# Kernel optimization log

Measured on AMD Instinct MI355X. Metric: run time of the kernel, lower is better.

## Reference

```python
import jax, jax.numpy as jnp
import numpy as np

D_MODEL = 256
D_STATE = 128          # d_model // 2
D_CONV = 4
EXPAND = 4
D_INNER = EXPAND * D_MODEL  # 1024
DT_RANK = (D_MODEL + 15) // 16  # 16
N_HEADS = 8
D_FF = 4 * D_MODEL
EPS = 1e-6


def layer_norm(x, a, b):
    # torch LayerNorm-like but with unbiased std (ddof=1) per the source
    mean = jnp.mean(x, axis=-1, keepdims=True)
    d = x.shape[-1]
    var = jnp.sum((x - mean) ** 2, axis=-1, keepdims=True) / (d - 1)
    std = jnp.sqrt(var)
    return a * (x - mean) / (std + EPS) + b


def silu(x):
    return x * jax.nn.sigmoid(x)


def mamba(x, in_proj_w, conv_w, conv_b, x_proj_w, dt_proj_w, dt_proj_b, A_log, Dp, out_proj_w):
    B, L, _ = x.shape
    xz = jnp.einsum('bld,ed->ble', x, in_proj_w)  # (B,L,2*D_INNER)
    xi, z = xz[..., :D_INNER], xz[..., D_INNER:]
    # causal depthwise conv1d over L
    xp = jnp.pad(xi, ((0, 0), (D_CONV - 1, 0), (0, 0)))
    u = conv_b
    for k in range(D_CONV):
        u = u + xp[:, k:k + L, :] * conv_w[:, k]
    u = silu(u)  # (B,L,D_INNER)
    dbl = jnp.einsum('bld,ed->ble', u, x_proj_w)  # (B,L,DT_RANK+2*D_STATE)
    dt = dbl[..., :DT_RANK]
    Bm = dbl[..., DT_RANK:DT_RANK + D_STATE]
    Cm = dbl[..., DT_RANK + D_STATE:]
    dt = jax.nn.softplus(jnp.einsum('blr,dr->bld', dt, dt_proj_w) + dt_proj_b)  # (B,L,D_INNER)
    A = -jnp.exp(A_log)  # (D_INNER, D_STATE)
    dA = jnp.exp(jnp.einsum('bld,dn->bldn', dt, A))          # (B,L,Din,N)
    dBu = jnp.einsum('bld,bln,bld->bldn', dt, Bm, u)          # (B,L,Din,N)

    def step(h, inp):
        dA_t, dBu_t, C_t = inp
        h = dA_t * h + dBu_t                    # (B,Din,N)
        y = jnp.einsum('bdn,bn->bd', h, C_t)    # (B,Din)
        return h, y

    h0 = jnp.zeros((B, D_INNER, D_STATE), dtype=x.dtype)
    _, ys = jax.lax.scan(step, h0, (jnp.swapaxes(dA, 0, 1), jnp.swapaxes(dBu, 0, 1), jnp.swapaxes(Cm, 0, 1)))
    y = jnp.swapaxes(ys, 0, 1) + u * Dp  # (B,L,Din)
    y = y * silu(z)
    return jnp.einsum('ble,de->bld', y, out_proj_w)


def cross_attention(q_in, kv_in, mask, wq_w, wq_b, wk_w, wk_b, wv_w, wv_b, wo_w, wo_b):
    B, Lq, _ = q_in.shape
    Lk = kv_in.shape[1]
    dk = D_MODEL // N_HEADS
    q = (jnp.einsum('bld,ed->ble', q_in, wq_w) + wq_b).reshape(B, Lq, N_HEADS, dk).transpose(0, 2, 1, 3)
    k = (jnp.einsum('bld,ed->ble', kv_in, wk_w) + wk_b).reshape(B, Lk, N_HEADS, dk).transpose(0, 2, 1, 3)
    v = (jnp.einsum('bld,ed->ble', kv_in, wv_w) + wv_b).reshape(B, Lk, N_HEADS, dk).transpose(0, 2, 1, 3)
    scores = jnp.einsum('bhqd,bhkd->bhqk', q, k) / np.sqrt(dk)
    # mask: (B,1,Lk) bool -> broadcast (B,1,1,Lk)
    scores = jnp.where(mask[:, None, :, :], scores, jnp.finfo(scores.dtype).min)
    p = jax.nn.softmax(scores, axis=-1)
    o = jnp.einsum('bhqk,bhkd->bhqd', p, v).transpose(0, 2, 1, 3).reshape(B, Lq, D_MODEL)
    return jnp.einsum('ble,de->bld', o, wo_w) + wo_b


def setup_inputs() -> dict:
    key = jax.random.key(0)
    ks = jax.random.split(key, 24)
    s = 0.02
    B, L, Lm = 2, 512, 512
    inp = {
        'x': jax.random.normal(ks[0], (B, L, D_MODEL), jnp.float32),
        'memory': jax.random.normal(ks[1], (B, Lm, D_MODEL), jnp.float32),
        'src_mask': jnp.ones((B, 1, Lm), bool),
        'tgt_mask': jnp.ones((B, 1, L), bool),
        # mamba params
        'in_proj_w': jax.random.normal(ks[2], (2 * D_INNER, D_MODEL)) * s,
        'conv_w': jax.random.normal(ks[3], (D_INNER, D_CONV)) * s,
        'conv_b': jnp.zeros((D_INNER,)),
        'x_proj_w': jax.random.normal(ks[4], (DT_RANK + 2 * D_STATE, D_INNER)) * s,
        'dt_proj_w': jax.random.normal(ks[5], (D_INNER, DT_RANK)) * s,
        'dt_proj_b': jnp.log(jnp.expm1(0.01)) * jnp.ones((D_INNER,)),
        'A_log': jnp.log(jnp.broadcast_to(jnp.arange(1, D_STATE + 1, dtype=jnp.float32), (D_INNER, D_STATE))),
        'Dp': jnp.ones((D_INNER,)),
        'out_proj_w': jax.random.normal(ks[6], (D_MODEL, D_INNER)) * s,
        # norms
        'norm1_a': jnp.ones((D_MODEL,)), 'norm1_b': jnp.zeros((D_MODEL,)),
        'norm2_a': jnp.ones((D_MODEL,)), 'norm2_b': jnp.zeros((D_MODEL,)),
        'norm3_a': jnp.ones((D_MODEL,)), 'norm3_b': jnp.zeros((D_MODEL,)),
        # cross attention
        'wq_w': jax.random.normal(ks[7], (D_MODEL, D_MODEL)) * s, 'wq_b': jnp.zeros((D_MODEL,)),
        'wk_w': jax.random.normal(ks[8], (D_MODEL, D_MODEL)) * s, 'wk_b': jnp.zeros((D_MODEL,)),
        'wv_w': jax.random.normal(ks[9], (D_MODEL, D_MODEL)) * s, 'wv_b': jnp.zeros((D_MODEL,)),
        'wo_w': jax.random.normal(ks[10], (D_MODEL, D_MODEL)) * s, 'wo_b': jnp.zeros((D_MODEL,)),
        # ffn
        'w1_w': jax.random.normal(ks[11], (D_FF, D_MODEL)) * s, 'w1_b': jnp.zeros((D_FF,)),
        'w2_w': jax.random.normal(ks[12], (D_MODEL, D_FF)) * s, 'w2_b': jnp.zeros((D_MODEL,)),
    }
    return inp


def reference(x, memory, src_mask, tgt_mask,
              in_proj_w, conv_w, conv_b, x_proj_w, dt_proj_w, dt_proj_b, A_log, Dp, out_proj_w,
              norm1_a, norm1_b, norm2_a, norm2_b, norm3_a, norm3_b,
              wq_w, wq_b, wk_w, wk_b, wv_w, wv_b, wo_w, wo_b,
              w1_w, w1_b, w2_w, w2_b):
    # self mamba block (pre-norm, residual); dropout = 0
    h = x + mamba(layer_norm(x, norm1_a, norm1_b), in_proj_w, conv_w, conv_b,
                  x_proj_w, dt_proj_w, dt_proj_b, A_log, Dp, out_proj_w)
    # cross attention block
    h = h + cross_attention(layer_norm(h, norm2_a, norm2_b), memory, src_mask,
                            wq_w, wq_b, wk_w, wk_b, wv_w, wv_b, wo_w, wo_b)
    # ffn block
    hn = layer_norm(h, norm3_a, norm3_b)
    ff = jnp.einsum('blf,df->bld', jax.nn.relu(jnp.einsum('bld,fd->blf', hn, w1_w) + w1_b), w2_w) + w2_b
    return h + ff
```

## Files before the change

kernel.cpp:

```cpp
#include <hip/hip_runtime.h>
#include <hip/hip_bf16.h>

#define B_SZ 2
#define L_SEQ 512
#define D_MODEL 256
#define D_STATE 128
#define D_CONV 4
#define D_INNER 1024
#define DT_RANK 16
#define N_HEADS 8
#define DK 32
#define D_FF 1024
#define R_TOT (B_SZ * L_SEQ)
#define DBL_LD (DT_RANK + 2 * D_STATE)
#define NSEG 16
#define SEGL 32
#define DPB 4

typedef __hip_bfloat16 bf16;
typedef __attribute__((ext_vector_type(8))) short short8;
typedef __attribute__((ext_vector_type(4))) float floatx4;

__device__ inline float fexp(float x) { return __expf(x); }
__device__ inline float fexp2(float x) { return __builtin_amdgcn_exp2f(x); }
__device__ inline float frcp(float x) { return __builtin_amdgcn_rcpf(x); }
__device__ inline float silu_f(float x) { return x * frcp(1.f + fexp(-x)); }
__device__ inline float softplus_f(float x) { return (x > 20.f) ? x : __logf(1.f + fexp(x)); }
__device__ inline float bf2f(unsigned short u) { return __uint_as_float(((unsigned)u) << 16); }

__device__ inline float dpp_sum64(float x) {
    x += __int_as_float(__builtin_amdgcn_update_dpp(0, __float_as_int(x), 0x111, 0xf, 0xf, true));
    x += __int_as_float(__builtin_amdgcn_update_dpp(0, __float_as_int(x), 0x112, 0xf, 0xf, true));
    x += __int_as_float(__builtin_amdgcn_update_dpp(0, __float_as_int(x), 0x114, 0xf, 0xf, true));
    x += __int_as_float(__builtin_amdgcn_update_dpp(0, __float_as_int(x), 0x118, 0xf, 0xf, true));
    x += __int_as_float(__builtin_amdgcn_update_dpp(0, __float_as_int(x), 0x142, 0xf, 0xf, true));
    x += __int_as_float(__builtin_amdgcn_update_dpp(0, __float_as_int(x), 0x143, 0xf, 0xf, true));
    return x;
}

__device__ inline float swz_xor16(float x) {
    return __int_as_float(__builtin_amdgcn_ds_swizzle(__float_as_int(x), 0x401F));
}
__device__ inline float swz_xor8(float x) {
    return __int_as_float(__builtin_amdgcn_ds_swizzle(__float_as_int(x), 0x201F));
}

#define S_MEM 262144
#define S_INW 524288
#define S_XPW 278528
#define S_OPW 262144
#define S_WQ  65536
#define S_WK  65536
#define S_WV  65536
#define S_WO  65536
#define S_W1  262144
#define S_W2  262144
#define S_TOT (S_MEM+S_INW+S_XPW+S_OPW+S_WQ+S_WK+S_WV+S_WO+S_W1+S_W2)
#define PACK_BLKS ((S_TOT + 255) / 256)
#define Z1_F4 (4 * R_TOT * D_MODEL / 4)
#define Z2_F4 (R_TOT * D_MODEL / 4)
#define Z3_F4 (R_TOT * DBL_LD / 4)
#define ZERO_BLKS ((Z1_F4 + Z2_F4 + Z3_F4 + 255) / 256)

__global__ __launch_bounds__(256) void pack_ln1(
    const float* __restrict__ s0, const float* __restrict__ s1,
    const float* __restrict__ s2, const float* __restrict__ s3,
    const float* __restrict__ s4, const float* __restrict__ s5,
    const float* __restrict__ s6, const float* __restrict__ s7,
    const float* __restrict__ s8, const float* __restrict__ s9,
    bf16* __restrict__ dst,
    const float* __restrict__ X, const float* __restrict__ a,
    const float* __restrict__ bvec, bf16* __restrict__ ln1b,
    float* __restrict__ zero1, float* __restrict__ zero2,
    float* __restrict__ zero3)
{
    __shared__ float r1[256], r2[256];
    if (blockIdx.x < PACK_BLKS) {
        const long i = (long)blockIdx.x * 256 + threadIdx.x;
        if (i >= S_TOT) return;
        const long off[11] = {0, S_MEM, S_MEM+S_INW, S_MEM+S_INW+S_XPW,
            S_MEM+S_INW+S_XPW+S_OPW, S_MEM+S_INW+S_XPW+S_OPW+S_WQ,
            S_MEM+S_INW+S_XPW+S_OPW+S_WQ+S_WK,
            S_MEM+S_INW+S_XPW+S_OPW+S_WQ+S_WK+S_WV,
            S_MEM+S_INW+S_XPW+S_OPW+S_WQ+S_WK+S_WV+S_WO,
            S_MEM+S_INW+S_XPW+S_OPW+S_WQ+S_WK+S_WV+S_WO+S_W1, S_TOT};
        const float* srcs[10] = {s0,s1,s2,s3,s4,s5,s6,s7,s8,s9};
        int seg = 0;
#pragma unroll
        for (int k = 1; k < 10; ++k) if (i >= off[k]) seg = k;
        dst[i] = __float2bfloat16(srcs[seg][i - off[seg]]);
    } else if (blockIdx.x < PACK_BLKS + R_TOT) {
        const int row = blockIdx.x - PACK_BLKS;
        const int t = threadIdx.x;
        const float v = X[(long)row * D_MODEL + t];
        r1[t] = v;
        r2[t] = v * v;
        __syncthreads();
        for (int s = 128; s > 0; s >>= 1) {
            if (t < s) { r1[t] += r1[t + s]; r2[t] += r2[t + s]; }
            __syncthreads();
        }
        const float mean = r1[0] * (1.f / 256.f);
        const float var = (r2[0] - 256.f * mean * mean) * (1.f / 255.f);
        const float sd = sqrtf(fmaxf(var, 0.f));
        const float o = a[t] * (v - mean) / (sd + 1e-6f) + bvec[t];
        ln1b[(long)row * D_MODEL + t] = __float2bfloat16(o);
    } else {
        const long i4 = (long)(blockIdx.x - PACK_BLKS - R_TOT) * 256 + threadIdx.x;
        const float4 z = {0.f, 0.f, 0.f, 0.f};
        if (i4 < Z1_F4)                      *(float4*)&zero1[i4 * 4] = z;
        else if (i4 < Z1_F4 + Z2_F4)          *(float4*)&zero2[(i4 - Z1_F4) * 4] = z;
        else if (i4 < Z1_F4 + Z2_F4 + Z3_F4)  *(float4*)&zero3[(i4 - Z1_F4 - Z2_F4) * 4] = z;
    }
}

template <int EPI>
__global__ __launch_bounds__(256) void mfma_gemm(
    const bf16* __restrict__ A, const bf16* __restrict__ W, int K,
    float* __restrict__ C, bf16* __restrict__ Cb, int ldc,
    const float* __restrict__ bias, const float* __restrict__ res,
    int M, int N)
{
    const int wave = threadIdx.x >> 6;
    const int lane = threadIdx.x & 63;
    const int row16 = lane & 15;
    const int quad  = lane >> 4;
    const int bm = blockIdx.y * 64 + wave * 16;
    const int bn = blockIdx.x * 64;

    floatx4 acc[4];
#pragma unroll
    for (int t = 0; t < 4; ++t) acc[t] = (floatx4){0.f, 0.f, 0.f, 0.f};

    const long arow = (long)(bm + row16) * K;
    for (int k0 = 0; k0 < K; k0 += 32) {
        const short8 av = *(const short8*)(A + arow + k0 + quad * 8);
#pragma unroll
        for (int t = 0; t < 4; ++t) {
            const int gn = bn + t * 16 + row16;
            short8 bv = {0,0,0,0,0,0,0,0};
            if (gn < N) bv = *(const short8*)(W + (long)gn * K + k0 + quad * 8);
            acc[t] = __builtin_amdgcn_mfma_f32_16x16x32_bf16(av, bv, acc[t], 0, 0, 0);
        }
    }

#pragma unroll
    for (int t = 0; t < 4; ++t) {
        const int gn = bn + t * 16 + row16;
        if (gn >= N) continue;
        const float bs = bias ? bias[gn] : 0.f;
#pragma unroll
        for (int r = 0; r < 4; ++r) {
            const int gm = bm + quad * 4 + r;
            float v = acc[t][r] + bs;
            if (EPI == 1) v = fmaxf(v, 0.f);
            const long ci = (long)gm * ldc + gn;
            if (res) v += res[ci];
            if (C)  C[ci] = v;
            if (Cb) Cb[ci] = __float2bfloat16(v);
        }
    }
}

template <int SK>
__global__ __launch_bounds__(256) void splitk_gemm(
    const bf16* __restrict__ A, const bf16* __restrict__ W, int K,
    float* __restrict__ C, int ldc,
    const float* __restrict__ bias, const float* __restrict__ res,
    int M, int N)
{
    const int wave = threadIdx.x >> 6;
    const int lane = threadIdx.x & 63;
    const int row16 = lane & 15;
    const int quad  = lane >> 4;
    const int bm = blockIdx.y * 64 + wave * 16;
    const int bn = blockIdx.x * 64;
    const int kz = blockIdx.z;
    const int ksl = K / SK;
    const int kbeg = kz * ksl;

    floatx4 acc[4];
#pragma unroll
    for (int t = 0; t < 4; ++t) acc[t] = (floatx4){0.f, 0.f, 0.f, 0.f};

    const long arow = (long)(bm + row16) * K;
    for (int k0 = kbeg; k0 < kbeg + ksl; k0 += 32) {
        const short8 av = *(const short8*)(A + arow + k0 + quad * 8);
#pragma unroll
        for (int t = 0; t < 4; ++t) {
            const int gn = bn + t * 16 + row16;
            short8 bv = {0,0,0,0,0,0,0,0};
            if (gn < N) bv = *(const short8*)(W + (long)gn * K + k0 + quad * 8);
            acc[t] = __builtin_amdgcn_mfma_f32_16x16x32_bf16(av, bv, acc[t], 0, 0, 0);
        }
    }

#pragma unroll
    for (int t = 0; t < 4; ++t) {
        const int gn = bn + t * 16 + row16;
        if (gn >= N) continue;
        const float bs = (kz == 0 && bias) ? bias[gn] : 0.f;
#pragma unroll
        for (int r = 0; r < 4; ++r) {
            const int gm = bm + quad * 4 + r;
            float v = acc[t][r] + bs;
            const long ci = (long)gm * ldc + gn;
            if (kz == 0 && res) v += res[ci];
            atomicAdd(&C[ci], v);
        }
    }
}

__global__ __launch_bounds__(256) void xproj_kv_gemm(
    const bf16* __restrict__ ub, const bf16* __restrict__ XPWb,
    float* __restrict__ dbl,
    const bf16* __restrict__ memb, const bf16* __restrict__ WKb,
    const bf16* __restrict__ WVb,
    const float* __restrict__ WKB, const float* __restrict__ WVB,
    float* __restrict__ kb, float* __restrict__ vb)
{
    const int wave = threadIdx.x >> 6;
    const int lane = threadIdx.x & 63;
    const int row16 = lane & 15;
    const int quad  = lane >> 4;
    const int bm = blockIdx.y * 64 + wave * 16;
    const int bn = blockIdx.x * 64;
    const int z = blockIdx.z;

    const bf16* A; const bf16* W; const float* bias; float* C;
    int K, N, ldc, kbeg, ksl;
    if (z < 4) {
        A = ub; W = XPWb; bias = nullptr; C = dbl;
        K = D_INNER; N = DBL_LD; ldc = DBL_LD;
        ksl = D_INNER / 4; kbeg = z * ksl;
    } else {
        if (bn >= D_MODEL) return;
        const int zz = z - 4;
        const int which = zz >> 1;
        const int kz = zz & 1;
        A = memb; W = which ? WVb : WKb;
        bias = (kz == 0) ? (which ? WVB : WKB) : nullptr;
        C = which ? vb : kb;
        K = D_MODEL; N = D_MODEL; ldc = D_MODEL;
        ksl = D_MODEL / 2; kbeg = kz * ksl;
    }

    floatx4 acc[4];
#pragma unroll
    for (int t = 0; t < 4; ++t) acc[t] = (floatx4){0.f, 0.f, 0.f, 0.f};

    const long arow = (long)(bm + row16) * K;
    for (int k0 = kbeg; k0 < kbeg + ksl; k0 += 32) {
        const short8 av = *(const short8*)(A + arow + k0 + quad * 8);
#pragma unroll
        for (int t = 0; t < 4; ++t) {
            const int gn = bn + t * 16 + row16;
            short8 bv = {0,0,0,0,0,0,0,0};
            if (gn < N) bv = *(const short8*)(W + (long)gn * K + k0 + quad * 8);
            acc[t] = __builtin_amdgcn_mfma_f32_16x16x32_bf16(av, bv, acc[t], 0, 0, 0);
        }
    }

#pragma unroll
    for (int t = 0; t < 4; ++t) {
        const int gn = bn + t * 16 + row16;
        if (gn >= N) continue;
        const float bs = bias ? bias[gn] : 0.f;
#pragma unroll
        for (int r = 0; r < 4; ++r) {
            const int gm = bm + quad * 4 + r;
            atomicAdd(&C[(long)gm * ldc + gn], acc[t][r] + bs);
        }
    }
}

__global__ __launch_bounds__(256) void q_gemm(
    const bf16* __restrict__ ln2b, const bf16* __restrict__ WQb,
    const float* __restrict__ WQB, float* __restrict__ qb)
{
    const int wave = threadIdx.x >> 6;
    const int lane = threadIdx.x & 63;
    const int row16 = lane & 15;
    const int quad  = lane >> 4;
    const int bm = blockIdx.y * 64 + wave * 16;
    const int bn = blockIdx.x * 64;
    const int kz = blockIdx.z;
    const int kbeg = kz * (D_MODEL / 2);

    floatx4 acc[4];
#pragma unroll
    for (int t = 0; t < 4; ++t) acc[t] = (floatx4){0.f, 0.f, 0.f, 0.f};

    const long arow = (long)(bm + row16) * D_MODEL;
    for (int k0 = kbeg; k0 < kbeg + D_MODEL / 2; k0 += 32) {
        const short8 av = *(const short8*)(ln2b + arow + k0 + quad * 8);
#pragma unroll
        for (int t = 0; t < 4; ++t) {
            const int gn = bn + t * 16 + row16;
            const short8 bv = *(const short8*)(WQb + (long)gn * D_MODEL + k0 + quad * 8);
            acc[t] = __builtin_amdgcn_mfma_f32_16x16x32_bf16(av, bv, acc[t], 0, 0, 0);
        }
    }
#pragma unroll
    for (int t = 0; t < 4; ++t) {
        const int gn = bn + t * 16 + row16;
        const float bs = (kz == 0) ? WQB[gn] : 0.f;
#pragma unroll
        for (int r = 0; r < 4; ++r) {
            const int gm = bm + quad * 4 + r;
            atomicAdd(&qb[(long)gm * D_MODEL + gn], acc[t][r] + bs);
        }
    }
}

__global__ __launch_bounds__(256) void gemm16_ln(
    const bf16* __restrict__ A, const bf16* __restrict__ W, int K,
    const float* __restrict__ bias, const float* __restrict__ res,
    float* __restrict__ Cf,
    const float* __restrict__ lna, const float* __restrict__ lnb,
    bf16* __restrict__ lnout)
{
    __shared__ float tile[16][264];
    __shared__ float red1[16][16];
    __shared__ float red2[16][16];
    const int w = threadIdx.x >> 6;
    const int lane = threadIdx.x & 63;
    const int row16 = lane & 15;
    const int quad  = lane >> 4;
    const int bm = blockIdx.x * 16;

    floatx4 acc[4];
#pragma unroll
    for (int t = 0; t < 4; ++t) acc[t] = (floatx4){0.f, 0.f, 0.f, 0.f};

    const long arow = (long)(bm + row16) * K;
    for (int k0 = 0; k0 < K; k0 += 32) {
        const short8 av = *(const short8*)(A + arow + k0 + quad * 8);
#pragma unroll
        for (int t = 0; t < 4; ++t) {
            const int gn = w * 64 + t * 16 + row16;
            const short8 bv = *(const short8*)(W + (long)gn * K + k0 + quad * 8);
            acc[t] = __builtin_amdgcn_mfma_f32_16x16x32_bf16(av, bv, acc[t], 0, 0, 0);
        }
    }

#pragma unroll
    for (int t = 0; t < 4; ++t) {
        const int gn = w * 64 + t * 16 + row16;
        const float bs = bias ? bias[gn] : 0.f;
#pragma unroll
        for (int r = 0; r < 4; ++r) {
            const int gm = bm + quad * 4 + r;
            float v = acc[t][r] + bs;
            const long ci = (long)gm * D_MODEL + gn;
            if (res) v += res[ci];
            Cf[ci] = v;
            tile[quad * 4 + r][gn] = v;
        }
    }
    __syncthreads();

    const int r = threadIdx.x >> 4;
    const int g = threadIdx.x & 15;
    float s = 0.f, q = 0.f;
#pragma unroll
    for (int i = 0; i < 16; ++i) {
        const float x = tile[r][g * 16 + i];
        s += x; q += x * x;
    }
    red1[r][g] = s; red2[r][g] = q;
    __syncthreads();
    float ts = 0.f, tq = 0.f;
#pragma unroll
    for (int i = 0; i < 16; ++i) { ts += red1[r][i]; tq += red2[r][i]; }
    const float mean = ts * (1.f / 256.f);
    const float var = (tq - 256.f * mean * mean) * (1.f / 255.f);
    const float sd = sqrtf(fmaxf(var, 0.f));
    const long rowbase = (long)(bm + r) * D_MODEL;
#pragma unroll
    for (int i = 0; i < 16; ++i) {
        const int c = g * 16 + i;
        const float o = lna[c] * (tile[r][c] - mean) / (sd + 1e-6f) + lnb[c];
        lnout[rowbase + c] = __float2bfloat16(o);
    }
}

__global__ __launch_bounds__(256) void ln_kernel(
    const float* __restrict__ x, const float* __restrict__ a,
    const float* __restrict__ bvec, bf16* __restrict__ out)
{
    const int row = blockIdx.x;
    const int t = threadIdx.x;
    const float v = x[(long)row * D_MODEL + t];
    __shared__ float r1[256], r2[256];
    r1[t] = v;
    r2[t] = v * v;
    __syncthreads();
    for (int s = 128; s > 0; s >>= 1) {
        if (t < s) { r1[t] += r1[t + s]; r2[t] += r2[t + s]; }
        __syncthreads();
    }
    const float mean = r1[0] * (1.f / 256.f);
    const float var = (r2[0] - 256.f * mean * mean) * (1.f / 255.f);
    const float sd = sqrtf(fmaxf(var, 0.f));
    const float o = a[t] * (v - mean) / (sd + 1e-6f) + bvec[t];
    out[(long)row * D_MODEL + t] = __float2bfloat16(o);
}

__global__ __launch_bounds__(256) void dt_gemm_T(
    const float* __restrict__ A , const float* __restrict__ W ,
    const float* __restrict__ bias, float* __restrict__ dtT)
{
    __shared__ float As[DT_RANK][65];
    __shared__ float Bs[DT_RANK][65];
    __shared__ float Ct[64][65];
    const int bm = blockIdx.y * 64;
    const int bn = blockIdx.x * 64;
    const int tid = threadIdx.x;
    const int tx = tid & 15;
    const int ty = tid >> 4;
    const int r = tid >> 2;
    const int kk = (tid & 3) * 4;
#pragma unroll
    for (int q = 0; q < 4; ++q) {
        As[kk + q][r] = A[(long)(bm + r) * DBL_LD + kk + q];
        Bs[kk + q][r] = W[(long)(bn + r) * DT_RANK + kk + q];
    }
    __syncthreads();
    float acc[4][4] = {};
#pragma unroll
    for (int k = 0; k < DT_RANK; ++k) {
        float a[4], bv[4];
#pragma unroll
        for (int i = 0; i < 4; ++i) a[i] = As[k][ty * 4 + i];
#pragma unroll
        for (int j = 0; j < 4; ++j) bv[j] = Bs[k][tx * 4 + j];
#pragma unroll
        for (int i = 0; i < 4; ++i)
#pragma unroll
            for (int j = 0; j < 4; ++j)
                acc[i][j] = fmaf(a[i], bv[j], acc[i][j]);
    }
#pragma unroll
    for (int i = 0; i < 4; ++i)
#pragma unroll
        for (int j = 0; j < 4; ++j)
            Ct[tx * 4 + j][ty * 4 + i] = softplus_f(acc[i][j] + bias[bn + tx * 4 + j]);
    __syncthreads();
    const int b = bm >> 9;
    const int l0 = bm & 511;
    const int r2 = tid >> 4;
    const int c4 = (tid & 15) * 4;
#pragma unroll
    for (int q = 0; q < 4; ++q) {
        const int dl = r2 + q * 16;
        float4 v = {Ct[dl][c4], Ct[dl][c4 + 1], Ct[dl][c4 + 2], Ct[dl][c4 + 3]};
        *(float4*)&dtT[((long)(b * D_INNER + bn + dl) << 9) + l0 + c4] = v;
    }
}

__global__ __launch_bounds__(256) void conv_silu_T(
    const bf16* __restrict__ xz, const float* __restrict__ cw,
    const float* __restrict__ cb, bf16* __restrict__ ub, float* __restrict__ uT)
{
    __shared__ float t[64][65];
    const int db = blockIdx.x;
    const int lb = blockIdx.y;
    const int b  = blockIdx.z;
    const int tid = threadIdx.x;
    const int r  = tid >> 4;
    const int c4 = (tid & 15) * 4;
    const int d0 = db * 64 + c4;

    const float4 cb4 = *(const float4*)&cb[d0];
    float cwa[4][4];
#pragma unroll
    for (int i = 0; i < 4; ++i) {
        const float4 w = *(const float4*)&cw[(d0 + i) * 4];
        cwa[i][0] = w.x; cwa[i][1] = w.y; cwa[i][2] = w.z; cwa[i][3] = w.w;
    }

#pragma unroll
    for (int q = 0; q < 4; ++q) {
        const int ll = r + q * 16;
        const int l = lb * 64 + ll;
        float s0 = cb4.x, s1 = cb4.y, s2 = cb4.z, s3 = cb4.w;
#pragma unroll
        for (int k = 0; k < D_CONV; ++k) {
            const int ls = l - 3 + k;
            if (ls >= 0) {
                const ushort4 xv = *(const ushort4*)&xz[((long)(b * L_SEQ + ls)) * (2 * D_INNER) + d0];
                s0 = fmaf(bf2f(xv.x), cwa[0][k], s0);
                s1 = fmaf(bf2f(xv.y), cwa[1][k], s1);
                s2 = fmaf(bf2f(xv.z), cwa[2][k], s2);
                s3 = fmaf(bf2f(xv.w), cwa[3][k], s3);
            }
        }
        s0 = silu_f(s0); s1 = silu_f(s1); s2 = silu_f(s2); s3 = silu_f(s3);
        bf16 b0 = __float2bfloat16(s0), b1 = __float2bfloat16(s1);
        bf16 b2 = __float2bfloat16(s2), b3 = __float2bfloat16(s3);
        ushort4 pk;
        pk.x = *reinterpret_cast<unsigned short*>(&b0);
        pk.y = *reinterpret_cast<unsigned short*>(&b1);
        pk.z = *reinterpret_cast<unsigned short*>(&b2);
        pk.w = *reinterpret_cast<unsigned short*>(&b3);
        *reinterpret_cast<ushort4*>(ub + ((long)(b * L_SEQ + l)) * D_INNER + d0) = pk;
        t[c4 + 0][ll] = s0; t[c4 + 1][ll] = s1;
        t[c4 + 2][ll] = s2; t[c4 + 3][ll] = s3;
    }
    __syncthreads();
#pragma unroll
    for (int q = 0; q < 4; ++q) {
        const int dl = r + q * 16;
        float4 v = {t[dl][c4], t[dl][c4 + 1], t[dl][c4 + 2], t[dl][c4 + 3]};
        *(float4*)&uT[((long)(b * D_INNER + db * 64 + dl) << 9) + lb * 64 + c4] = v;
    }
}

__global__ __launch_bounds__(1024) void scan_fused(
    const float* __restrict__ dtT, const float* __restrict__ uT,
    const float* __restrict__ dbl, const float* __restrict__ A_log,
    float* __restrict__ ysT)
{
    const int b  = blockIdx.x >> 8;
    const int d0 = (blockIdx.x & 255) * DPB;
    const int w = threadIdx.x >> 6;
    const int lane = threadIdx.x & 63;
    const int n0 = lane * 2;

    __shared__ float Sh[NSEG][DPB][D_STATE];
    __shared__ float Ph[NSEG][DPB][D_STATE];

    float An0[DPB], An1[DPB];
#pragma unroll
    for (int di = 0; di < DPB; ++di) {
        An0[di] = -fexp(A_log[(long)(d0 + di) * D_STATE + n0]) * 1.44269504f;
        An1[di] = -fexp(A_log[(long)(d0 + di) * D_STATE + n0 + 1]) * 1.44269504f;
    }

    const float* blp = dbl + ((long)(b * L_SEQ + w * SEGL)) * DBL_LD + DT_RANK + n0;
    const float* clp = blp + D_STATE;
    const long tbase = ((long)(b * D_INNER + d0) << 9) + w * SEGL;

    if (w < NSEG - 1) {
        float h0[DPB] = {}, h1[DPB] = {}, sdt[DPB] = {};
        for (int s = 0; s < SEGL / 8; ++s) {
            float2 Bv[8];
#pragma unroll
            for (int j = 0; j < 8; ++j)
                Bv[j] = *(const float2*)(blp + (long)(s * 8 + j) * DBL_LD);
#pragma unroll
            for (int di = 0; di < DPB; ++di) {
                const float* dtp = dtT + tbase + ((long)di << 9) + s * 8;
                const float* up  = uT  + tbase + ((long)di << 9) + s * 8;
                const float4 dt0 = *(const float4*)dtp;
                const float4 dt1 = *(const float4*)(dtp + 4);
                const float4 u0  = *(const float4*)up;
                const float4 u1  = *(const float4*)(up + 4);
                const float dts[8] = {dt0.x, dt0.y, dt0.z, dt0.w, dt1.x, dt1.y, dt1.z, dt1.w};
                const float us[8]  = {u0.x,  u0.y,  u0.z,  u0.w,  u1.x,  u1.y,  u1.z,  u1.w};
#pragma unroll
                for (int j = 0; j < 8; ++j) {
                    const float dtv = dts[j];
                    sdt[di] += dtv;
                    const float dtu = dtv * us[j];
                    h0[di] = fmaf(fexp2(dtv * An0[di]), h0[di], dtu * Bv[j].x);
                    h1[di] = fmaf(fexp2(dtv * An1[di]), h1[di], dtu * Bv[j].y);
                }
            }
        }
#pragma unroll
        for (int di = 0; di < DPB; ++di) {
            Sh[w][di][n0]     = h0[di];
            Sh[w][di][n0 + 1] = h1[di];
            Ph[w][di][n0]     = fexp2(An0[di] * sdt[di]);
            Ph[w][di][n0 + 1] = fexp2(An1[di] * sdt[di]);
        }
    }
    __syncthreads();

    float h0[DPB] = {}, h1[DPB] = {};
    for (int s = 0; s < w; ++s) {
#pragma unroll
        for (int di = 0; di < DPB; ++di) {
            h0[di] = fmaf(Ph[s][di][n0],     h0[di], Sh[s][di][n0]);
            h1[di] = fmaf(Ph[s][di][n0 + 1], h1[di], Sh[s][di][n0 + 1]);
        }
    }

    const int bpa = (lane ^ 32) << 2;
    const bool lo32 = lane < 32;
    const bool b16 = (lane & 16) != 0;
    const bool b8  = (lane & 8) != 0;
    const int g = lane >> 3;
    const bool wl = (lane & 7) == 7;

    for (int s = 0; s < SEGL / 8; ++s) {
        float2 Bv[8], Cv[8];
#pragma unroll
        for (int j = 0; j < 8; ++j) {
            Bv[j] = *(const float2*)(blp + (long)(s * 8 + j) * DBL_LD);
            Cv[j] = *(const float2*)(clp + (long)(s * 8 + j) * DBL_LD);
        }
#pragma unroll
        for (int di = 0; di < DPB; ++di) {
            const float* dtp = dtT + tbase + ((long)di << 9) + s * 8;
            const float* up  = uT  + tbase + ((long)di << 9) + s * 8;
            const float4 dt0 = *(const float4*)dtp;
            const float4 dt1 = *(const float4*)(dtp + 4);
            const float4 u0  = *(const float4*)up;
            const float4 u1  = *(const float4*)(up + 4);
            const float dts[8] = {dt0.x, dt0.y, dt0.z, dt0.w, dt1.x, dt1.y, dt1.z, dt1.w};
            const float us[8]  = {u0.x,  u0.y,  u0.z,  u0.w,  u1.x,  u1.y,  u1.z,  u1.w};
            float yp[8];
#pragma unroll
            for (int j = 0; j < 8; ++j) {
                const float dtv = dts[j];
                const float dtu = dtv * us[j];
                h0[di] = fmaf(fexp2(dtv * An0[di]), h0[di], dtu * Bv[j].x);
                h1[di] = fmaf(fexp2(dtv * An1[di]), h1[di], dtu * Bv[j].y);
                yp[j] = fmaf(h0[di], Cv[j].x, h1[di] * Cv[j].y);
            }
            float z0[4];
#pragma unroll
            for (int j = 0; j < 4; ++j) {
                const float t = lo32 ? yp[j]     : yp[j + 4];
                const float u = lo32 ? yp[j + 4] : yp[j];
                z0[j] = t + __int_as_float(
                    __builtin_amdgcn_ds_bpermute(bpa, __float_as_int(u)));
            }
            float z1[2];
#pragma unroll
            for (int j = 0; j < 2; ++j) {
                const float t = b16 ? z0[j + 2] : z0[j];
                const float u = b16 ? z0[j]     : z0[j + 2];
                z1[j] = t + swz_xor16(u);
            }
            float z2;
            {
                const float t = b8 ? z1[1] : z1[0];
                const float u = b8 ? z1[0] : z1[1];
                z2 = t + swz_xor8(u);
            }
            z2 += __int_as_float(__builtin_amdgcn_update_dpp(0, __float_as_int(z2), 0x111, 0xf, 0xf, true));
            z2 += __int_as_float(__builtin_amdgcn_update_dpp(0, __float_as_int(z2), 0x112, 0xf, 0xf, true));
            z2 += __int_as_float(__builtin_amdgcn_update_dpp(0, __float_as_int(z2), 0x114, 0xf, 0xf, true));
            if (wl) ysT[tbase + ((long)di << 9) + s * 8 + g] = z2;
        }
    }
}

__global__ __launch_bounds__(256) void gate_kernel(
    const float* __restrict__ ysT, const float* __restrict__ uT,
    const float* __restrict__ Dp, const bf16* __restrict__ xz,
    bf16* __restrict__ y)
{
    __shared__ float t[64][65];
    __shared__ float t2[64][65];
    const int db = blockIdx.x;
    const int lb = blockIdx.y;
    const int b  = blockIdx.z;
    const int tid = threadIdx.x;
    const int r  = tid >> 4;
    const int c4 = (tid & 15) * 4;

#pragma unroll
    for (int q = 0; q < 4; ++q) {
        const int dr = r + q * 16;
        const long base = (((long)(b * D_INNER + db * 64 + dr)) << 9) + lb * 64 + c4;
        const float4 v = *(const float4*)&ysT[base];
        const float4 w = *(const float4*)&uT[base];
        t[dr][c4 + 0] = v.x; t[dr][c4 + 1] = v.y;
        t[dr][c4 + 2] = v.z; t[dr][c4 + 3] = v.w;
        t2[dr][c4 + 0] = w.x; t2[dr][c4 + 1] = w.y;
        t2[dr][c4 + 2] = w.z; t2[dr][c4 + 3] = w.w;
    }
    __syncthreads();

    const float4 dp4 = *(const float4*)&Dp[db * 64 + c4];
#pragma unroll
    for (int q = 0; q < 4; ++q) {
        const int lr = r + q * 16;
        const long row = (long)b * L_SEQ + lb * 64 + lr;
        const ushort4 zu = *(const ushort4*)&xz[row * 2 * D_INNER + D_INNER + db * 64 + c4];
        const float r0 = (t[c4 + 0][lr] + t2[c4 + 0][lr] * dp4.x) * silu_f(bf2f(zu.x));
        const float r1 = (t[c4 + 1][lr] + t2[c4 + 1][lr] * dp4.y) * silu_f(bf2f(zu.y));
        const float r2 = (t[c4 + 2][lr] + t2[c4 + 2][lr] * dp4.z) * silu_f(bf2f(zu.z));
        const float r3 = (t[c4 + 3][lr] + t2[c4 + 3][lr] * dp4.w) * silu_f(bf2f(zu.w));
        bf16 b0 = __float2bfloat16(r0), b1 = __float2bfloat16(r1);
        bf16 b2 = __float2bfloat16(r2), b3 = __float2bfloat16(r3);
        ushort4 pk;
        pk.x = *reinterpret_cast<unsigned short*>(&b0);
        pk.y = *reinterpret_cast<unsigned short*>(&b1);
        pk.z = *reinterpret_cast<unsigned short*>(&b2);
        pk.w = *reinterpret_cast<unsigned short*>(&b3);
        *reinterpret_cast<ushort4*>(y + row * D_INNER + db * 64 + c4) = pk;
    }
}

#define QT 16
#define CK 64

__global__ __launch_bounds__(256) void attn_kernel(
    const float* __restrict__ q, const float* __restrict__ k,
    const float* __restrict__ v, bf16* __restrict__ o)
{
    const int qt = blockIdx.x;
    const int hh = blockIdx.y;
    const int b  = blockIdx.z;
    const int t = threadIdx.x;
    const int lane = t & 15;
    const int qa = t >> 4;
    const int q0 = qt * QT + qa;

    __shared__ float Ks[CK][36];
    __shared__ float Vs[CK][36];

    const float scale = 0.17677669529663687f;
    float qr0[32];
    {
        const float* q0p = q + ((long)(b * L_SEQ + q0) * D_MODEL + hh * DK);
#pragma unroll
        for (int i = 0; i < 8; ++i) {
            const float4 a = *(const float4*)&q0p[i * 4];
            qr0[i*4+0] = a.x * scale; qr0[i*4+1] = a.y * scale;
            qr0[i*4+2] = a.z * scale; qr0[i*4+3] = a.w * scale;
        }
    }

    float m0 = -1e30f, l0 = 0.f, o0[32] = {};

    for (int c = 0; c < L_SEQ; c += CK) {
        __syncthreads();
        {
            const int fid = t * 2;
            const int row = fid >> 3;
            const int c0  = (fid & 7) * 4;
            const float* kp = k + ((long)(b * L_SEQ + c + row) * D_MODEL + hh * DK + c0);
            const float* vp = v + ((long)(b * L_SEQ + c + row) * D_MODEL + hh * DK + c0);
            *(float4*)&Ks[row][c0]     = *(const float4*)kp;
            *(float4*)&Ks[row][c0 + 4] = *(const float4*)(kp + 4);
            *(float4*)&Vs[row][c0]     = *(const float4*)vp;
            *(float4*)&Vs[row][c0 + 4] = *(const float4*)(vp + 4);
        }
        __syncthreads();

        float s0[4];
#pragma unroll
        for (int i = 0; i < 4; ++i) {
            const int kk = i * 16 + lane;
            float a0 = 0.f;
#pragma unroll
            for (int dd = 0; dd < 32; dd += 4) {
                const float4 kv = *(const float4*)&Ks[kk][dd];
                a0 = fmaf(qr0[dd+0], kv.x, a0); a0 = fmaf(qr0[dd+1], kv.y, a0);
                a0 = fmaf(qr0[dd+2], kv.z, a0); a0 = fmaf(qr0[dd+3], kv.w, a0);
            }
            s0[i] = a0;
        }

        float cm0 = s0[0];
#pragma unroll
        for (int i = 1; i < 4; ++i) cm0 = fmaxf(cm0, s0[i]);
#pragma unroll
        for (int off = 8; off > 0; off >>= 1)
            cm0 = fmaxf(cm0, __shfl_down(cm0, off, 16));
        cm0 = __shfl(cm0, 0, 16);

        const float nm0 = fmaxf(m0, cm0);
        const float al0 = fexp(m0 - nm0);
        l0 *= al0;
#pragma unroll
        for (int dd = 0; dd < 32; ++dd) o0[dd] *= al0;
        m0 = nm0;

        float p0[4];
#pragma unroll
        for (int i = 0; i < 4; ++i) { p0[i] = fexp(s0[i] - m0); l0 += p0[i]; }

#pragma unroll
        for (int i = 0; i < 4; ++i) {
            const int kk = i * 16 + lane;
#pragma unroll
            for (int dd = 0; dd < 32; dd += 4) {
                const float4 vv = *(const float4*)&Vs[kk][dd];
                o0[dd+0] = fmaf(p0[i], vv.x, o0[dd+0]);
                o0[dd+1] = fmaf(p0[i], vv.y, o0[dd+1]);
                o0[dd+2] = fmaf(p0[i], vv.z, o0[dd+2]);
                o0[dd+3] = fmaf(p0[i], vv.w, o0[dd+3]);
            }
        }
    }

#pragma unroll
    for (int off = 8; off > 0; off >>= 1) {
        l0 += __shfl_down(l0, off, 16);
#pragma unroll
        for (int dd = 0; dd < 32; ++dd) o0[dd] += __shfl_down(o0[dd], off, 16);
    }
    if (lane == 0) {
        const float i0 = 1.f / l0;
        bf16* op0 = o + ((long)(b * L_SEQ + q0) * D_MODEL + hh * DK);
#pragma unroll
        for (int dd = 0; dd < 32; ++dd) op0[dd] = __float2bfloat16(o0[dd] * i0);
    }
}


extern "C" void kernel_launch(void* const* d_in, const int* in_sizes, int n_in,
                              void* d_out, int out_size, void* d_ws, size_t ws_size,
                              hipStream_t stream) {
    const float* X   = (const float*)d_in[0];
    const float* MEM = (const float*)d_in[1];
    const float* CW  = (const float*)d_in[5];
    const float* CB  = (const float*)d_in[6];
    const float* DTW = (const float*)d_in[8];
    const float* DTB = (const float*)d_in[9];
    const float* ALG = (const float*)d_in[10];
    const float* DP  = (const float*)d_in[11];
    const float* N1A = (const float*)d_in[13];
    const float* N1B = (const float*)d_in[14];
    const float* N2A = (const float*)d_in[15];
    const float* N2B = (const float*)d_in[16];
    const float* N3A = (const float*)d_in[17];
    const float* N3B = (const float*)d_in[18];
    const float* WQB = (const float*)d_in[20];
    const float* WKB = (const float*)d_in[22];
    const float* WVB = (const float*)d_in[24];
    const float* WOB = (const float*)d_in[26];
    const float* W1B = (const float*)d_in[28];
    const float* W2B = (const float*)d_in[30];
    const float* INW = (const float*)d_in[4];
    const float* XPW = (const float*)d_in[7];
    const float* OPW = (const float*)d_in[12];
    const float* WQ  = (const float*)d_in[19];
    const float* WKw = (const float*)d_in[21];
    const float* WVw = (const float*)d_in[23];
    const float* WO  = (const float*)d_in[25];
    const float* W1  = (const float*)d_in[27];
    const float* W2  = (const float*)d_in[29];
    float* out = (float*)d_out;

    bf16* bp = (bf16*)d_ws;
    bf16* ub   = bp;  bp += (long)R_TOT * D_INNER;
    bf16* ybb  = bp;  bp += (long)R_TOT * D_INNER;
    bf16* ffab = ybb;
    bf16* xzb  = bp;  bp += (long)R_TOT * 2 * D_INNER;
    bf16* ln1b = bp;  bp += (long)R_TOT * D_MODEL;
    bf16* aob  = ln1b;
    bf16* ln2b = bp;  bp += (long)R_TOT * D_MODEL;
    bf16* ln3b = ln2b;
    bf16* arena = bp; bp += S_TOT;
    bf16* MEMb = arena;
    bf16* INWb = MEMb + S_MEM;
    bf16* XPWb = INWb + S_INW;
    bf16* OPWb = XPWb + S_XPW;
    bf16* WQb  = OPWb + S_OPW;
    bf16* WKb  = WQb + S_WQ;
    bf16* WVb  = WKb + S_WK;
    bf16* WOb  = WVb + S_WV;
    bf16* W1b  = WOb + S_WO;
    bf16* W2b  = W1b + S_W1;

    float* p = (float*)(bp + ((((long)(bp - (bf16*)d_ws)) & 1) ? 1 : 0));
    float* uT  = p;                                  p += (long)R_TOT * D_INNER;
    float* dbl = p;                                  p += (long)R_TOT * DBL_LD;
    float* dtT = p;                                  p += (long)R_TOT * D_INNER;
    float* ysT = p;                                  p += (long)R_TOT * D_INNER;
    float* h1  = p;                                  p += (long)R_TOT * D_MODEL;
    float* qb  = p;                                  p += (long)R_TOT * D_MODEL;
    float* kb  = p;                                  p += (long)R_TOT * D_MODEL;
    float* vb  = p;                                  p += (long)R_TOT * D_MODEL;
    float* h2  = p;                                  p += (long)R_TOT * D_MODEL;

    const dim3 blk256(256);
    const int MT64 = R_TOT / 64;

    pack_ln1<<<PACK_BLKS + R_TOT + ZERO_BLKS, blk256, 0, stream>>>(
        MEM, INW, XPW, OPW, WQ, WKw, WVw, WO, W1, W2, arena,
        X, N1A, N1B, ln1b, h1, out, dbl);

    mfma_gemm<0><<<dim3(2 * D_INNER / 64, MT64), blk256, 0, stream>>>(
        ln1b, INWb, D_MODEL, nullptr, xzb, 2 * D_INNER, nullptr, nullptr,
        R_TOT, 2 * D_INNER);

    conv_silu_T<<<dim3(D_INNER / 64, L_SEQ / 64, B_SZ), blk256, 0, stream>>>(
        xzb, CW, CB, ub, uT);

    xproj_kv_gemm<<<dim3((DBL_LD + 63) / 64, MT64, 8), blk256, 0, stream>>>(
        ub, XPWb, dbl, MEMb, WKb, WVb, WKB, WVB, kb, vb);

    dt_gemm_T<<<dim3(D_INNER / 64, MT64), blk256, 0, stream>>>(dbl, DTW, DTB, dtT);

    scan_fused<<<B_SZ * D_INNER / DPB, dim3(1024), 0, stream>>>(dtT, uT, dbl, ALG, ysT);

    gate_kernel<<<dim3(D_INNER / 64, L_SEQ / 64, B_SZ), blk256, 0, stream>>>(
        ysT, uT, DP, xzb, ybb);

    splitk_gemm<4><<<dim3(D_MODEL / 64, MT64, 4), blk256, 0, stream>>>(
        ybb, OPWb, D_INNER, h1, D_MODEL, nullptr, X, R_TOT, D_MODEL);

    ln_kernel<<<R_TOT, blk256, 0, stream>>>(h1, N2A, N2B, ln2b);

    q_gemm<<<dim3(D_MODEL / 64, MT64, 2), blk256, 0, stream>>>(ln2b, WQb, WQB, qb);

    attn_kernel<<<dim3(L_SEQ / QT, N_HEADS, B_SZ), blk256, 0, stream>>>(qb, kb, vb, aob);

    gemm16_ln<<<R_TOT / 16, blk256, 0, stream>>>(
        aob, WOb, D_MODEL, WOB, h1, h2, N3A, N3B, ln3b);

    mfma_gemm<1><<<dim3(D_FF / 64, MT64), blk256, 0, stream>>>(
        ln3b, W1b, D_MODEL, nullptr, ffab, D_FF, W1B, nullptr, R_TOT, D_FF);

    splitk_gemm<4><<<dim3(D_MODEL / 64, MT64, 4), blk256, 0, stream>>>(
        ffab, W2b, D_FF, out, D_MODEL, W2B, h2, R_TOT, D_MODEL);

    (void)in_sizes; (void)n_in; (void)out_size; (void)ws_size;
}
```

Measured before the change: 321.8 us.

## Fuse gating into scan, out-proj with LN2, and Q projection into attention

The D-skip and SiLU(z) gating move into the scan kernel's epilogue, so the ysT intermediate and the separate gate kernel go away. The out_proj GEMM plus LayerNorm2 now use the fused gemm16_ln kernel in place of the split-K atomic GEMM and a standalone LN kernel. The Q projection is computed per block inside the attention kernel with scalar FMAs, which removes q_gemm and the qb buffer. This cuts launches and intermediate traffic, but each attention block recomputes Q on scalar ALUs and gemm16_ln now runs with K=1024 on only 64 blocks.

```diff
diff --git a/kernel.cpp b/kernel.cpp
--- a/kernel.cpp
+++ b/kernel.cpp
@@ -28,16 +28,6 @@
 __device__ inline float softplus_f(float x) { return (x > 20.f) ? x : __logf(1.f + fexp(x)); }
 __device__ inline float bf2f(unsigned short u) { return __uint_as_float(((unsigned)u) << 16); }
 
-__device__ inline float dpp_sum64(float x) {
-    x += __int_as_float(__builtin_amdgcn_update_dpp(0, __float_as_int(x), 0x111, 0xf, 0xf, true));
-    x += __int_as_float(__builtin_amdgcn_update_dpp(0, __float_as_int(x), 0x112, 0xf, 0xf, true));
-    x += __int_as_float(__builtin_amdgcn_update_dpp(0, __float_as_int(x), 0x114, 0xf, 0xf, true));
-    x += __int_as_float(__builtin_amdgcn_update_dpp(0, __float_as_int(x), 0x118, 0xf, 0xf, true));
-    x += __int_as_float(__builtin_amdgcn_update_dpp(0, __float_as_int(x), 0x142, 0xf, 0xf, true));
-    x += __int_as_float(__builtin_amdgcn_update_dpp(0, __float_as_int(x), 0x143, 0xf, 0xf, true));
-    return x;
-}
-
 __device__ inline float swz_xor16(float x) {
     return __int_as_float(__builtin_amdgcn_ds_swizzle(__float_as_int(x), 0x401F));
 }
@@ -57,7 +47,7 @@
 #define S_W2  262144
 #define S_TOT (S_MEM+S_INW+S_XPW+S_OPW+S_WQ+S_WK+S_WV+S_WO+S_W1+S_W2)
 #define PACK_BLKS ((S_TOT + 255) / 256)
-#define Z1_F4 (4 * R_TOT * D_MODEL / 4)
+#define Z1_F4 (2 * R_TOT * D_MODEL / 4)
 #define Z2_F4 (R_TOT * D_MODEL / 4)
 #define Z3_F4 (R_TOT * DBL_LD / 4)
 #define ZERO_BLKS ((Z1_F4 + Z2_F4 + Z3_F4 + 255) / 256)
@@ -274,45 +264,6 @@
     }
 }
 
-__global__ __launch_bounds__(256) void q_gemm(
-    const bf16* __restrict__ ln2b, const bf16* __restrict__ WQb,
-    const float* __restrict__ WQB, float* __restrict__ qb)
-{
-    const int wave = threadIdx.x >> 6;
-    const int lane = threadIdx.x & 63;
-    const int row16 = lane & 15;
-    const int quad  = lane >> 4;
-    const int bm = blockIdx.y * 64 + wave * 16;
-    const int bn = blockIdx.x * 64;
-    const int kz = blockIdx.z;
-    const int kbeg = kz * (D_MODEL / 2);
-
-    floatx4 acc[4];
-#pragma unroll
-    for (int t = 0; t < 4; ++t) acc[t] = (floatx4){0.f, 0.f, 0.f, 0.f};
-
-    const long arow = (long)(bm + row16) * D_MODEL;
-    for (int k0 = kbeg; k0 < kbeg + D_MODEL / 2; k0 += 32) {
-        const short8 av = *(const short8*)(ln2b + arow + k0 + quad * 8);
-#pragma unroll
-        for (int t = 0; t < 4; ++t) {
-            const int gn = bn + t * 16 + row16;
-            const short8 bv = *(const short8*)(WQb + (long)gn * D_MODEL + k0 + quad * 8);
-            acc[t] = __builtin_amdgcn_mfma_f32_16x16x32_bf16(av, bv, acc[t], 0, 0, 0);
-        }
-    }
-#pragma unroll
-    for (int t = 0; t < 4; ++t) {
-        const int gn = bn + t * 16 + row16;
-        const float bs = (kz == 0) ? WQB[gn] : 0.f;
-#pragma unroll
-        for (int r = 0; r < 4; ++r) {
-            const int gm = bm + quad * 4 + r;
-            atomicAdd(&qb[(long)gm * D_MODEL + gn], acc[t][r] + bs);
-        }
-    }
-}
-
 __global__ __launch_bounds__(256) void gemm16_ln(
     const bf16* __restrict__ A, const bf16* __restrict__ W, int K,
     const float* __restrict__ bias, const float* __restrict__ res,
@@ -385,28 +336,6 @@
     }
 }
 
-__global__ __launch_bounds__(256) void ln_kernel(
-    const float* __restrict__ x, const float* __restrict__ a,
-    const float* __restrict__ bvec, bf16* __restrict__ out)
-{
-    const int row = blockIdx.x;
-    const int t = threadIdx.x;
-    const float v = x[(long)row * D_MODEL + t];
-    __shared__ float r1[256], r2[256];
-    r1[t] = v;
-    r2[t] = v * v;
-    __syncthreads();
-    for (int s = 128; s > 0; s >>= 1) {
-        if (t < s) { r1[t] += r1[t + s]; r2[t] += r2[t + s]; }
-        __syncthreads();
-    }
-    const float mean = r1[0] * (1.f / 256.f);
-    const float var = (r2[0] - 256.f * mean * mean) * (1.f / 255.f);
-    const float sd = sqrtf(fmaxf(var, 0.f));
-    const float o = a[t] * (v - mean) / (sd + 1e-6f) + bvec[t];
-    out[(long)row * D_MODEL + t] = __float2bfloat16(o);
-}
-
 __global__ __launch_bounds__(256) void dt_gemm_T(
     const float* __restrict__ A , const float* __restrict__ W ,
     const float* __restrict__ bias, float* __restrict__ dtT)
@@ -520,7 +449,8 @@
 __global__ __launch_bounds__(1024) void scan_fused(
     const float* __restrict__ dtT, const float* __restrict__ uT,
     const float* __restrict__ dbl, const float* __restrict__ A_log,
-    float* __restrict__ ysT)
+    const float* __restrict__ Dp, const bf16* __restrict__ xz,
+    bf16* __restrict__ yb)
 {
     const int b  = blockIdx.x >> 8;
     const int d0 = (blockIdx.x & 255) * DPB;
@@ -537,6 +467,8 @@
         An0[di] = -fexp(A_log[(long)(d0 + di) * D_STATE + n0]) * 1.44269504f;
         An1[di] = -fexp(A_log[(long)(d0 + di) * D_STATE + n0 + 1]) * 1.44269504f;
     }
+    const float4 dp4 = *(const float4*)&Dp[d0];
+    const float dpc[4] = {dp4.x, dp4.y, dp4.z, dp4.w};
 
     const float* blp = dbl + ((long)(b * L_SEQ + w * SEGL)) * DBL_LD + DT_RANK + n0;
     const float* clp = blp + D_STATE;
@@ -602,6 +534,7 @@
             Bv[j] = *(const float2*)(blp + (long)(s * 8 + j) * DBL_LD);
             Cv[j] = *(const float2*)(clp + (long)(s * 8 + j) * DBL_LD);
         }
+        float ysel[DPB];
 #pragma unroll
         for (int di = 0; di < DPB; ++di) {
             const float* dtp = dtT + tbase + ((long)di << 9) + s * 8;
@@ -645,56 +578,32 @@
             z2 += __int_as_float(__builtin_amdgcn_update_dpp(0, __float_as_int(z2), 0x111, 0xf, 0xf, true));
             z2 += __int_as_float(__builtin_amdgcn_update_dpp(0, __float_as_int(z2), 0x112, 0xf, 0xf, true));
             z2 += __int_as_float(__builtin_amdgcn_update_dpp(0, __float_as_int(z2), 0x114, 0xf, 0xf, true));
-            if (wl) ysT[tbase + ((long)di << 9) + s * 8 + g] = z2;
-        }
-    }
-}
-
-__global__ __launch_bounds__(256) void gate_kernel(
-    const float* __restrict__ ysT, const float* __restrict__ uT,
-    const float* __restrict__ Dp, const bf16* __restrict__ xz,
-    bf16* __restrict__ y)
-{
-    __shared__ float t[64][65];
-    __shared__ float t2[64][65];
-    const int db = blockIdx.x;
-    const int lb = blockIdx.y;
-    const int b  = blockIdx.z;
-    const int tid = threadIdx.x;
-    const int r  = tid >> 4;
-    const int c4 = (tid & 15) * 4;
-
-#pragma unroll
-    for (int q = 0; q < 4; ++q) {
-        const int dr = r + q * 16;
-        const long base = (((long)(b * D_INNER + db * 64 + dr)) << 9) + lb * 64 + c4;
-        const float4 v = *(const float4*)&ysT[base];
-        const float4 w = *(const float4*)&uT[base];
-        t[dr][c4 + 0] = v.x; t[dr][c4 + 1] = v.y;
-        t[dr][c4 + 2] = v.z; t[dr][c4 + 3] = v.w;
-        t2[dr][c4 + 0] = w.x; t2[dr][c4 + 1] = w.y;
-        t2[dr][c4 + 2] = w.z; t2[dr][c4 + 3] = w.w;
-    }
-    __syncthreads();
-
-    const float4 dp4 = *(const float4*)&Dp[db * 64 + c4];
-#pragma unroll
-    for (int q = 0; q < 4; ++q) {
-        const int lr = r + q * 16;
-        const long row = (long)b * L_SEQ + lb * 64 + lr;
-        const ushort4 zu = *(const ushort4*)&xz[row * 2 * D_INNER + D_INNER + db * 64 + c4];
-        const float r0 = (t[c4 + 0][lr] + t2[c4 + 0][lr] * dp4.x) * silu_f(bf2f(zu.x));
-        const float r1 = (t[c4 + 1][lr] + t2[c4 + 1][lr] * dp4.y) * silu_f(bf2f(zu.y));
-        const float r2 = (t[c4 + 2][lr] + t2[c4 + 2][lr] * dp4.z) * silu_f(bf2f(zu.z));
-        const float r3 = (t[c4 + 3][lr] + t2[c4 + 3][lr] * dp4.w) * silu_f(bf2f(zu.w));
-        bf16 b0 = __float2bfloat16(r0), b1 = __float2bfloat16(r1);
-        bf16 b2 = __float2bfloat16(r2), b3 = __float2bfloat16(r3);
-        ushort4 pk;
-        pk.x = *reinterpret_cast<unsigned short*>(&b0);
-        pk.y = *reinterpret_cast<unsigned short*>(&b1);
-        pk.z = *reinterpret_cast<unsigned short*>(&b2);
-        pk.w = *reinterpret_cast<unsigned short*>(&b3);
-        *reinterpret_cast<ushort4*>(y + row * D_INNER + db * 64 + c4) = pk;
+            const float t01 = (g & 1) ? us[1] : us[0];
+            const float t23 = (g & 1) ? us[3] : us[2];
+            const float t45 = (g & 1) ? us[5] : us[4];
+            const float t67 = (g & 1) ? us[7] : us[6];
+            const float t03 = (g & 2) ? t23 : t01;
+            const float t47 = (g & 2) ? t67 : t45;
+            const float ug  = (g & 4) ? t47 : t03;
+            ysel[di] = z2 + ug * dpc[di];
+        }
+        if (wl) {
+            const int l = w * SEGL + s * 8 + g;
+            const long row = (long)b * L_SEQ + l;
+            const ushort4 zu = *(const ushort4*)&xz[row * (2 * D_INNER) + D_INNER + d0];
+            const float y0 = ysel[0] * silu_f(bf2f(zu.x));
+            const float y1 = ysel[1] * silu_f(bf2f(zu.y));
+            const float y2 = ysel[2] * silu_f(bf2f(zu.z));
+            const float y3 = ysel[3] * silu_f(bf2f(zu.w));
+            bf16 o0 = __float2bfloat16(y0), o1 = __float2bfloat16(y1);
+            bf16 o2 = __float2bfloat16(y2), o3 = __float2bfloat16(y3);
+            ushort4 pk;
+            pk.x = *reinterpret_cast<unsigned short*>(&o0);
+            pk.y = *reinterpret_cast<unsigned short*>(&o1);
+            pk.z = *reinterpret_cast<unsigned short*>(&o2);
+            pk.w = *reinterpret_cast<unsigned short*>(&o3);
+            *reinterpret_cast<ushort4*>(yb + row * D_INNER + d0) = pk;
+        }
     }
 }
 
@@ -702,31 +611,52 @@
 #define CK 64
 
 __global__ __launch_bounds__(256) void attn_kernel(
-    const float* __restrict__ q, const float* __restrict__ k,
-    const float* __restrict__ v, bf16* __restrict__ o)
+    const bf16* __restrict__ ln2b, const bf16* __restrict__ WQb,
+    const float* __restrict__ WQB,
+    const float* __restrict__ k, const float* __restrict__ v,
+    bf16* __restrict__ o)
 {
     const int qt = blockIdx.x;
     const int hh = blockIdx.y;
     const int b  = blockIdx.z;
     const int t = threadIdx.x;
+
+    __shared__ float qs[QT][33];
+    __shared__ float Ks[CK][36];
+    __shared__ float Vs[CK][36];
+
+    {
+        const int qr = t >> 4;
+        const int c  = (t * 2) & 31;
+        const bf16* ar = ln2b + ((long)(b * L_SEQ + qt * QT + qr)) * D_MODEL;
+        const bf16* w0 = WQb + (long)(hh * DK + c) * D_MODEL;
+        const bf16* w1 = w0 + D_MODEL;
+        float a0 = 0.f, a1 = 0.f;
+        for (int kk = 0; kk < D_MODEL; kk += 4) {
+            const ushort4 av = *(const ushort4*)(ar + kk);
+            const ushort4 b0 = *(const ushort4*)(w0 + kk);
+            const ushort4 b1 = *(const ushort4*)(w1 + kk);
+            a0 = fmaf(bf2f(av.x), bf2f(b0.x), a0);
+            a0 = fmaf(bf2f(av.y), bf2f(b0.y), a0);
+            a0 = fmaf(bf2f(av.z), bf2f(b0.z), a0);
+            a0 = fmaf(bf2f(av.w), bf2f(b0.w), a0);
+            a1 = fmaf(bf2f(av.x), bf2f(b1.x), a1);
+            a1 = fmaf(bf2f(av.y), bf2f(b1.y), a1);
+            a1 = fmaf(bf2f(av.z), bf2f(b1.z), a1);
+            a1 = fmaf(bf2f(av.w), bf2f(b1.w), a1);
+        }
+        qs[qr][c]     = a0 + WQB[hh * DK + c];
+        qs[qr][c + 1] = a1 + WQB[hh * DK + c + 1];
+    }
+    __syncthreads();
+
     const int lane = t & 15;
     const int qa = t >> 4;
     const int q0 = qt * QT + qa;
-
-    __shared__ float Ks[CK][36];
-    __shared__ float Vs[CK][36];
-
     const float scale = 0.17677669529663687f;
     float qr0[32];
-    {
-        const float* q0p = q + ((long)(b * L_SEQ + q0) * D_MODEL + hh * DK);
-#pragma unroll
-        for (int i = 0; i < 8; ++i) {
-            const float4 a = *(const float4*)&q0p[i * 4];
-            qr0[i*4+0] = a.x * scale; qr0[i*4+1] = a.y * scale;
-            qr0[i*4+2] = a.z * scale; qr0[i*4+3] = a.w * scale;
-        }
-    }
+#pragma unroll
+    for (int i = 0; i < 32; ++i) qr0[i] = qs[qa][i] * scale;
 
     float m0 = -1e30f, l0 = 0.f, o0[32] = {};
 
@@ -866,11 +796,9 @@
     float* uT  = p;                                  p += (long)R_TOT * D_INNER;
     float* dbl = p;                                  p += (long)R_TOT * DBL_LD;
     float* dtT = p;                                  p += (long)R_TOT * D_INNER;
-    float* ysT = p;                                  p += (long)R_TOT * D_INNER;
-    float* h1  = p;                                  p += (long)R_TOT * D_MODEL;
-    float* qb  = p;                                  p += (long)R_TOT * D_MODEL;
     float* kb  = p;                                  p += (long)R_TOT * D_MODEL;
     float* vb  = p;                                  p += (long)R_TOT * D_MODEL;
+    float* h1  = p;                                  p += (long)R_TOT * D_MODEL;
     float* h2  = p;                                  p += (long)R_TOT * D_MODEL;
 
     const dim3 blk256(256);
@@ -878,7 +806,7 @@
 
     pack_ln1<<<PACK_BLKS + R_TOT + ZERO_BLKS, blk256, 0, stream>>>(
         MEM, INW, XPW, OPW, WQ, WKw, WVw, WO, W1, W2, arena,
-        X, N1A, N1B, ln1b, h1, out, dbl);
+        X, N1A, N1B, ln1b, kb, out, dbl);
 
     mfma_gemm<0><<<dim3(2 * D_INNER / 64, MT64), blk256, 0, stream>>>(
         ln1b, INWb, D_MODEL, nullptr, xzb, 2 * D_INNER, nullptr, nullptr,
@@ -892,19 +820,14 @@
 
     dt_gemm_T<<<dim3(D_INNER / 64, MT64), blk256, 0, stream>>>(dbl, DTW, DTB, dtT);
 
-    scan_fused<<<B_SZ * D_INNER / DPB, dim3(1024), 0, stream>>>(dtT, uT, dbl, ALG, ysT);
-
-    gate_kernel<<<dim3(D_INNER / 64, L_SEQ / 64, B_SZ), blk256, 0, stream>>>(
-        ysT, uT, DP, xzb, ybb);
-
-    splitk_gemm<4><<<dim3(D_MODEL / 64, MT64, 4), blk256, 0, stream>>>(
-        ybb, OPWb, D_INNER, h1, D_MODEL, nullptr, X, R_TOT, D_MODEL);
-
-    ln_kernel<<<R_TOT, blk256, 0, stream>>>(h1, N2A, N2B, ln2b);
-
-    q_gemm<<<dim3(D_MODEL / 64, MT64, 2), blk256, 0, stream>>>(ln2b, WQb, WQB, qb);
-
-    attn_kernel<<<dim3(L_SEQ / QT, N_HEADS, B_SZ), blk256, 0, stream>>>(qb, kb, vb, aob);
+    scan_fused<<<B_SZ * D_INNER / DPB, dim3(1024), 0, stream>>>(
+        dtT, uT, dbl, ALG, DP, xzb, ybb);
+
+    gemm16_ln<<<R_TOT / 16, blk256, 0, stream>>>(
+        ybb, OPWb, D_INNER, nullptr, X, h1, N2A, N2B, ln2b);
+
+    attn_kernel<<<dim3(L_SEQ / QT, N_HEADS, B_SZ), blk256, 0, stream>>>(
+        ln2b, WQb, WQB, kb, vb, aob);
 
     gemm16_ln<<<R_TOT / 16, blk256, 0, stream>>>(
         aob, WOb, D_MODEL, WOB, h1, h2, N3A, N3B, ln3b);
```

Measured after the change: 430.3 us. +33.7%, slower.
